# Performance work log

Measured on AMD Instinct MI355X. Metric: run time of the kernel, lower is better.

## Reference

```python
import jax, jax.numpy as jnp
import numpy as np
import math

EMBED = 1024
HEADS = 16
HEAD_DIM = EMBED // HEADS
WINDOW = 128
B, S = 2, 2048


def setup_inputs() -> dict:
    key = jax.random.key(0)
    k1, k2, k3, k4 = jax.random.split(key, 4)
    values = jax.random.normal(k1, (B, S, EMBED), dtype=jnp.float32)
    keys = jax.random.normal(k2, (B, S, EMBED), dtype=jnp.float32)
    queries = jax.random.normal(k3, (B, S, EMBED), dtype=jnp.float32)
    # sliding-window band mask: 1 where |i-j| <= WINDOW//2, else 0
    idx = jnp.arange(S)
    band = (jnp.abs(idx[:, None] - idx[None, :]) <= WINDOW // 2).astype(jnp.int32)
    mask = band[None, None, :, :]  # [1,1,S,S], broadcasts over batch and heads
    w_out = jax.random.normal(k4, (EMBED, EMBED), dtype=jnp.float32) * (1.0 / math.sqrt(EMBED))
    b_out = jnp.zeros((EMBED,), dtype=jnp.float32)
    return {"values": values, "keys": keys, "queries": queries, "mask": mask,
            "w_out": w_out, "b_out": b_out}


def reference(values, keys, queries, mask, w_out, b_out):
    N, q_len = queries.shape[0], queries.shape[1]
    v = values.reshape(N, -1, HEADS, HEAD_DIM)
    k = keys.reshape(N, -1, HEADS, HEAD_DIM)
    q = queries.reshape(N, -1, HEADS, HEAD_DIM)
    # dense N x N energy, as in the original (no windowed blocking)
    energy = jnp.einsum('nqhd,nkhd->nhqk', q, k)
    energy = jnp.where(mask == 0, jnp.float32(-1e20), energy)
    attn = jax.nn.softmax(energy / math.sqrt(EMBED), axis=3)
    out = jnp.einsum('nhql,nlhd->nqhd', attn, v).reshape(N, q_len, HEADS * HEAD_DIM)
    return out @ w_out.T + b_out
```

## Files before the change

### kernel.cpp

```cpp
#include <hip/hip_runtime.h>

typedef __bf16 bf16x8 __attribute__((ext_vector_type(8)));
typedef float floatx4 __attribute__((ext_vector_type(4)));
typedef unsigned short ushortx8 __attribute__((ext_vector_type(8)));
typedef unsigned short ushortx4 __attribute__((ext_vector_type(4)));
typedef unsigned short ushort_t;

#define SB 2048
#define EB 1024
#define HB 16
#define DB 64
#define QT 128
#define KB2 256
#define KROW 72
#define VROW 272
#define PROW 168

__device__ __forceinline__ ushort_t f2bf(float f) {
    union { float f; unsigned int u; } v; v.f = f;
    unsigned int r = v.u + 0x7fffu + ((v.u >> 16) & 1u);
    return (ushort_t)(r >> 16);
}

union BF8 { ushortx8 u; bf16x8 b; };

__global__ __launch_bounds__(256) void cvtw_kernel(const float* __restrict__ w,
                                                   ushort_t* __restrict__ wb) {
    int i = blockIdx.x * 256 + threadIdx.x;
    const float4 v = ((const float4*)w)[i];
    ushortx4 o;
    o.x = f2bf(v.x); o.y = f2bf(v.y); o.z = f2bf(v.z); o.w = f2bf(v.w);
    ((ushortx4*)wb)[i] = o;
}

__global__ __launch_bounds__(512) void attn_kernel(const float* __restrict__ Vg,
                                                   const float* __restrict__ Kg,
                                                   const float* __restrict__ Qg,
                                                   ushort_t* __restrict__ Xg) {
    __shared__ ushort_t KP[8 * 16 * PROW];
    __shared__ ushort_t Vt[DB * VROW];

    const int tid  = threadIdx.x;
    const int wave = tid >> 6;
    const int lane = tid & 63;
    const int l15  = lane & 15;
    const int l4   = lane >> 4;

    const int qt = blockIdx.x & 15;
    const int h  = (blockIdx.x >> 4) & 15;
    const int b  = blockIdx.x >> 8;

    const int q0     = qt * QT;
    const int kstart = q0 - 64;

    const float* Kbase = Kg + ((size_t)b * SB) * EB + h * DB;
    const float* Vbase = Vg + ((size_t)b * SB) * EB + h * DB;

    #pragma unroll
    for (int it = 0; it < (KB2 * DB / 4) / 512; ++it) {
        int idx = it * 512 + tid;
        int j   = idx >> 4;
        int d4  = (idx & 15) * 4;
        int kk  = kstart + j;
        float4 kv = make_float4(0.f, 0.f, 0.f, 0.f);
        float4 vv = make_float4(0.f, 0.f, 0.f, 0.f);
        if (kk >= 0 && kk < SB) {
            kv = *(const float4*)(Kbase + (size_t)kk * EB + d4);
            vv = *(const float4*)(Vbase + (size_t)kk * EB + d4);
        }
        ushortx4 ku;
        ku.x = f2bf(kv.x); ku.y = f2bf(kv.y); ku.z = f2bf(kv.z); ku.w = f2bf(kv.w);
        *(ushortx4*)(KP + j * KROW + d4) = ku;
        Vt[(d4 + 0) * VROW + j] = f2bf(vv.x);
        Vt[(d4 + 1) * VROW + j] = f2bf(vv.y);
        Vt[(d4 + 2) * VROW + j] = f2bf(vv.z);
        Vt[(d4 + 3) * VROW + j] = f2bf(vv.w);
    }
    {
        int r = tid >> 3, c = 256 + ((tid & 7) * 2);
        if (r < DB) { Vt[r * VROW + c] = 0; Vt[r * VROW + c + 1] = 0; }
    }

    const int qrow = q0 + wave * 16 + l15;
    const float* Qrow = Qg + ((size_t)b * SB + qrow) * EB + h * DB;
    bf16x8 qfrag[2];
    #pragma unroll
    for (int ks = 0; ks < 2; ++ks) {
        const float4* p = (const float4*)(Qrow + ks * 32 + l4 * 8);
        float4 a0 = p[0], a1 = p[1];
        BF8 t;
        t.u[0] = f2bf(a0.x); t.u[1] = f2bf(a0.y); t.u[2] = f2bf(a0.z); t.u[3] = f2bf(a0.w);
        t.u[4] = f2bf(a1.x); t.u[5] = f2bf(a1.y); t.u[6] = f2bf(a1.z); t.u[7] = f2bf(a1.w);
        qfrag[ks] = t.b;
    }

    __syncthreads();

    floatx4 sfrag[9];
    #pragma unroll
    for (int nt = 0; nt < 9; ++nt) {
        floatx4 acc = {0.f, 0.f, 0.f, 0.f};
        #pragma unroll
        for (int ks = 0; ks < 2; ++ks) {
            bf16x8 kf = *(const bf16x8*)(KP + (16 * (wave + nt) + l15) * KROW + ks * 32 + l4 * 8);
            acc = __builtin_amdgcn_mfma_f32_16x16x32_bf16(qfrag[ks], kf, acc, 0, 0, 0);
        }
        sfrag[nt] = acc;
    }

    const float scale2 = 0.04508421903306637f;
    #pragma unroll
    for (int nt = 0; nt < 9; ++nt) {
        int key = kstart + 16 * (wave + nt) + l15;
        #pragma unroll
        for (int r = 0; r < 4; ++r) {
            int m = l4 * 4 + r;
            int d = 16 * nt + l15 - m;
            bool valid = (d >= 0) && (d <= 128) && (key >= 0) && (key < SB);
            float s = sfrag[nt][r] * scale2;
            sfrag[nt][r] = valid ? s : -1e30f;
        }
    }
    #pragma unroll
    for (int r = 0; r < 4; ++r) {
        float mx = -1e30f;
        #pragma unroll
        for (int nt = 0; nt < 9; ++nt) mx = fmaxf(mx, sfrag[nt][r]);
        mx = fmaxf(mx, __shfl_xor(mx, 1));
        mx = fmaxf(mx, __shfl_xor(mx, 2));
        mx = fmaxf(mx, __shfl_xor(mx, 4));
        mx = fmaxf(mx, __shfl_xor(mx, 8));
        float sum = 0.f;
        #pragma unroll
        for (int nt = 0; nt < 9; ++nt) {
            float e = exp2f(sfrag[nt][r] - mx);
            sfrag[nt][r] = e;
            sum += e;
        }
        sum += __shfl_xor(sum, 1);
        sum += __shfl_xor(sum, 2);
        sum += __shfl_xor(sum, 4);
        sum += __shfl_xor(sum, 8);
        float inv = 1.f / sum;
        #pragma unroll
        for (int nt = 0; nt < 9; ++nt) sfrag[nt][r] *= inv;
    }

    __syncthreads();
    ushort_t* Pw = KP + wave * (16 * PROW);
    #pragma unroll
    for (int nt = 0; nt < 9; ++nt)
        #pragma unroll
        for (int r = 0; r < 4; ++r)
            Pw[(l4 * 4 + r) * PROW + nt * 16 + l15] = f2bf(sfrag[nt][r]);
    #pragma unroll
    for (int r = 0; r < 4; ++r) {
        int row = l4 * 4 + r;
        if (l15 < 12) {
            Pw[row * PROW + 144 + l15 * 2]     = 0;
            Pw[row * PROW + 144 + l15 * 2 + 1] = 0;
        }
    }
    __syncthreads();

    #pragma unroll
    for (int nt = 0; nt < 4; ++nt) {
        floatx4 acc = {0.f, 0.f, 0.f, 0.f};
        #pragma unroll
        for (int ks = 0; ks < 5; ++ks) {
            bf16x8 pf = *(const bf16x8*)(Pw + l15 * PROW + ks * 32 + l4 * 8);
            bf16x8 vf = *(const bf16x8*)(Vt + (nt * 16 + l15) * VROW + 16 * wave + ks * 32 + l4 * 8);
            acc = __builtin_amdgcn_mfma_f32_16x16x32_bf16(pf, vf, acc, 0, 0, 0);
        }
        #pragma unroll
        for (int r = 0; r < 4; ++r) {
            int q  = q0 + wave * 16 + l4 * 4 + r;
            int dd = h * DB + nt * 16 + l15;
            Xg[((size_t)b * SB + q) * EB + dd] = f2bf(acc[r]);
        }
    }
}

__device__ __forceinline__ void async_load16(const void* g, void* l) {
    __builtin_amdgcn_global_load_lds((__attribute__((address_space(1))) void*)g,
                                     (__attribute__((address_space(3))) void*)l,
                                     16, 0, 0);
}

__global__ __launch_bounds__(256) void proj_kernel(const ushort_t* __restrict__ X,
                                                   const ushort_t* __restrict__ Wb,
                                                   const float* __restrict__ bias,
                                                   float* __restrict__ out) {
    __shared__ ushort_t As[64 * 32];
    __shared__ ushort_t Bs[128 * 32];

    const int tid  = threadIdx.x;
    const int wave = tid >> 6;
    const int lane = tid & 63;
    const int l15  = lane & 15;
    const int l4   = lane >> 4;

    const int m0 = blockIdx.x * 64;
    const int n0 = blockIdx.y * 128;
    const int wm = (wave >> 1) * 32;
    const int wn = (wave & 1) * 64;

    floatx4 acc[2][4];
    #pragma unroll
    for (int i = 0; i < 2; ++i)
        #pragma unroll
        for (int j = 0; j < 4; ++j)
            acc[i][j] = (floatx4){0.f, 0.f, 0.f, 0.f};

    const int cA  = wave * 64 + lane;
    const int cB0 = wave * 128 + lane;
    const ushort_t* gA  = X  + (size_t)(m0 + (cA >> 2)) * EB + (cA & 3) * 8;
    const ushort_t* gB0 = Wb + (size_t)(n0 + (cB0 >> 2)) * EB + (cB0 & 3) * 8;
    const ushort_t* gB1 = Wb + (size_t)(n0 + ((cB0 + 64) >> 2)) * EB + ((cB0 + 64) & 3) * 8;
    ushort_t* lA  = As + wave * 512;
    ushort_t* lB0 = Bs + wave * 1024;
    ushort_t* lB1 = Bs + wave * 1024 + 512;

    for (int kt = 0; kt < EB / 32; ++kt) {
        async_load16(gA,  lA);
        async_load16(gB0, lB0);
        async_load16(gB1, lB1);
        gA += 32; gB0 += 32; gB1 += 32;
        __syncthreads();

        bf16x8 af[2], bfr[4];
        #pragma unroll
        for (int i = 0; i < 2; ++i)
            af[i] = *(const bf16x8*)(As + (wm + i * 16 + l15) * 32 + l4 * 8);
        #pragma unroll
        for (int j = 0; j < 4; ++j)
            bfr[j] = *(const bf16x8*)(Bs + (wn + j * 16 + l15) * 32 + l4 * 8);
        #pragma unroll
        for (int i = 0; i < 2; ++i)
            #pragma unroll
            for (int j = 0; j < 4; ++j)
                acc[i][j] = __builtin_amdgcn_mfma_f32_16x16x32_bf16(af[i], bfr[j], acc[i][j], 0, 0, 0);
        __syncthreads();
    }

    #pragma unroll
    for (int i = 0; i < 2; ++i)
        #pragma unroll
        for (int j = 0; j < 4; ++j)
            #pragma unroll
            for (int r = 0; r < 4; ++r) {
                int row = m0 + wm + i * 16 + l4 * 4 + r;
                int col = n0 + wn + j * 16 + l15;
                out[(size_t)row * EB + col] = acc[i][j][r] + bias[col];
            }
}

extern "C" void kernel_launch(void* const* d_in, const int* in_sizes, int n_in,
                              void* d_out, int out_size, void* d_ws, size_t ws_size,
                              hipStream_t stream) {
    const float* values  = (const float*)d_in[0];
    const float* keys    = (const float*)d_in[1];
    const float* queries = (const float*)d_in[2];
    const float* w_out   = (const float*)d_in[4];
    const float* b_out   = (const float*)d_in[5];
    float* out = (float*)d_out;

    ushort_t* Xb = (ushort_t*)d_ws;
    ushort_t* Wb = (ushort_t*)d_ws + (size_t)4096 * 1024;

    cvtw_kernel<<<(EB * EB / 4) / 256, 256, 0, stream>>>(w_out, Wb);
    attn_kernel<<<2 * HB * (SB / QT), 512, 0, stream>>>(values, keys, queries, Xb);
    proj_kernel<<<dim3(4096 / 64, EB / 128), 256, 0, stream>>>(Xb, Wb, b_out, out);
}
```

Before: 137.2 us.

## Swizzle V tile in LDS, stage attention output through LDS, retile projection GEMM

The attention kernel now XOR-swizzles the transposed V tile in LDS to cut bank conflicts. It also stages each block's output in LDS so it can be written to global memory as coalesced 16-byte stores instead of scattered 2-byte stores. The projection GEMM is retiled to 128x64 tiles with 2 waves, each computing a 64x64 sub-tile, and uses a 64-wide K step with swizzled async LDS loads to cut bank conflicts and barrier count. The trade-off is fewer threads per block, more registers per wave and lower occupancy in the GEMM.

```diff
diff --git a/kernel.cpp b/kernel.cpp
--- a/kernel.cpp
+++ b/kernel.cpp
@@ -15,6 +15,7 @@
 #define KROW 72
 #define VROW 272
 #define PROW 168
+#define XROW 72
 
 __device__ __forceinline__ ushort_t f2bf(float f) {
     union { float f; unsigned int u; } v; v.f = f;
@@ -71,10 +72,11 @@
         ushortx4 ku;
         ku.x = f2bf(kv.x); ku.y = f2bf(kv.y); ku.z = f2bf(kv.z); ku.w = f2bf(kv.w);
         *(ushortx4*)(KP + j * KROW + d4) = ku;
-        Vt[(d4 + 0) * VROW + j] = f2bf(vv.x);
-        Vt[(d4 + 1) * VROW + j] = f2bf(vv.y);
-        Vt[(d4 + 2) * VROW + j] = f2bf(vv.z);
-        Vt[(d4 + 3) * VROW + j] = f2bf(vv.w);
+        int cs = ((((j >> 3) ^ (l15 & 7)) << 3) | (j & 7));
+        Vt[(d4 + 0) * VROW + cs] = f2bf(vv.x);
+        Vt[(d4 + 1) * VROW + cs] = f2bf(vv.y);
+        Vt[(d4 + 2) * VROW + cs] = f2bf(vv.z);
+        Vt[(d4 + 3) * VROW + cs] = f2bf(vv.w);
     }
     {
         int r = tid >> 3, c = 256 + ((tid & 7) * 2);
@@ -161,23 +163,38 @@
             Pw[row * PROW + 144 + l15 * 2 + 1] = 0;
         }
     }
-    __syncthreads();
-
+
+    floatx4 oacc[4];
     #pragma unroll
     for (int nt = 0; nt < 4; ++nt) {
         floatx4 acc = {0.f, 0.f, 0.f, 0.f};
+        int dsw = (nt * 4 + (l15 >> 2)) & 7;
         #pragma unroll
         for (int ks = 0; ks < 5; ++ks) {
+            int col = 16 * wave + ks * 32 + l4 * 8;
+            int c   = col >> 3;
+            int coff = (c < 32) ? ((c ^ dsw) << 3) : (c << 3);
             bf16x8 pf = *(const bf16x8*)(Pw + l15 * PROW + ks * 32 + l4 * 8);
-            bf16x8 vf = *(const bf16x8*)(Vt + (nt * 16 + l15) * VROW + 16 * wave + ks * 32 + l4 * 8);
+            bf16x8 vf = *(const bf16x8*)(Vt + (nt * 16 + l15) * VROW + coff);
             acc = __builtin_amdgcn_mfma_f32_16x16x32_bf16(pf, vf, acc, 0, 0, 0);
         }
-        #pragma unroll
-        for (int r = 0; r < 4; ++r) {
-            int q  = q0 + wave * 16 + l4 * 4 + r;
-            int dd = h * DB + nt * 16 + l15;
-            Xg[((size_t)b * SB + q) * EB + dd] = f2bf(acc[r]);
-        }
+        oacc[nt] = acc;
+    }
+
+    __syncthreads();
+    ushort_t* Xs = KP;
+    #pragma unroll
+    for (int nt = 0; nt < 4; ++nt)
+        #pragma unroll
+        for (int r = 0; r < 4; ++r)
+            Xs[(wave * 16 + l4 * 4 + r) * XROW + nt * 16 + l15] = f2bf(oacc[nt][r]);
+    __syncthreads();
+    #pragma unroll
+    for (int it = 0; it < 2; ++it) {
+        int idx = it * 512 + tid;
+        int row = idx >> 3, ch = idx & 7;
+        bf16x8 val = *(const bf16x8*)(Xs + row * XROW + ch * 8);
+        *(bf16x8*)(Xg + ((size_t)b * SB + q0 + row) * EB + h * DB + ch * 8) = val;
     }
 }
 
@@ -187,12 +204,12 @@
                                      16, 0, 0);
 }
 
-__global__ __launch_bounds__(256) void proj_kernel(const ushort_t* __restrict__ X,
+__global__ __launch_bounds__(128) void proj_kernel(const ushort_t* __restrict__ X,
                                                    const ushort_t* __restrict__ Wb,
                                                    const float* __restrict__ bias,
                                                    float* __restrict__ out) {
-    __shared__ ushort_t As[64 * 32];
-    __shared__ ushort_t Bs[128 * 32];
+    __shared__ ushort_t As[128 * 64];
+    __shared__ ushort_t Bs[64 * 64];
 
     const int tid  = threadIdx.x;
     const int wave = tid >> 6;
@@ -200,59 +217,62 @@
     const int l15  = lane & 15;
     const int l4   = lane >> 4;
 
-    const int m0 = blockIdx.x * 64;
-    const int n0 = blockIdx.y * 128;
-    const int wm = (wave >> 1) * 32;
-    const int wn = (wave & 1) * 64;
-
-    floatx4 acc[2][4];
-    #pragma unroll
-    for (int i = 0; i < 2; ++i)
+    const int m0 = blockIdx.x * 128;
+    const int n0 = blockIdx.y * 64;
+    const int wm = wave * 64;
+
+    floatx4 acc[4][4];
+    #pragma unroll
+    for (int i = 0; i < 4; ++i)
         #pragma unroll
         for (int j = 0; j < 4; ++j)
             acc[i][j] = (floatx4){0.f, 0.f, 0.f, 0.f};
 
-    const int cA  = wave * 64 + lane;
-    const int cB0 = wave * 128 + lane;
-    const ushort_t* gA  = X  + (size_t)(m0 + (cA >> 2)) * EB + (cA & 3) * 8;
-    const ushort_t* gB0 = Wb + (size_t)(n0 + (cB0 >> 2)) * EB + (cB0 & 3) * 8;
-    const ushort_t* gB1 = Wb + (size_t)(n0 + ((cB0 + 64) >> 2)) * EB + ((cB0 + 64) & 3) * 8;
-    ushort_t* lA  = As + wave * 512;
-    ushort_t* lB0 = Bs + wave * 1024;
-    ushort_t* lB1 = Bs + wave * 1024 + 512;
-
-    for (int kt = 0; kt < EB / 32; ++kt) {
-        async_load16(gA,  lA);
-        async_load16(gB0, lB0);
-        async_load16(gB1, lB1);
-        gA += 32; gB0 += 32; gB1 += 32;
+    const int kc8 = (((tid & 7) ^ ((tid >> 3) & 7)) << 3);
+    const ushort_t* gA = X  + (size_t)(m0 + (tid >> 3)) * EB + kc8;
+    const ushort_t* gB = Wb + (size_t)(n0 + (tid >> 3)) * EB + kc8;
+    ushort_t* lA = As + wave * 512;
+    ushort_t* lB = Bs + wave * 512;
+
+    for (int kt = 0; kt < EB / 64; ++kt) {
+        #pragma unroll
+        for (int p = 0; p < 8; ++p) async_load16(gA + (size_t)p * 16 * EB, lA + p * 1024);
+        #pragma unroll
+        for (int p = 0; p < 4; ++p) async_load16(gB + (size_t)p * 16 * EB, lB + p * 1024);
+        gA += 64; gB += 64;
         __syncthreads();
 
-        bf16x8 af[2], bfr[4];
-        #pragma unroll
-        for (int i = 0; i < 2; ++i)
-            af[i] = *(const bf16x8*)(As + (wm + i * 16 + l15) * 32 + l4 * 8);
-        #pragma unroll
-        for (int j = 0; j < 4; ++j)
-            bfr[j] = *(const bf16x8*)(Bs + (wn + j * 16 + l15) * 32 + l4 * 8);
-        #pragma unroll
-        for (int i = 0; i < 2; ++i)
+        #pragma unroll
+        for (int ks = 0; ks < 2; ++ks) {
+            const int sw = (((ks * 4 + l4) ^ (l15 & 7)) << 3);
+            bf16x8 af[4], bfr[4];
+            #pragma unroll
+            for (int i = 0; i < 4; ++i)
+                af[i] = *(const bf16x8*)(As + (wm + i * 16 + l15) * 64 + sw);
             #pragma unroll
             for (int j = 0; j < 4; ++j)
-                acc[i][j] = __builtin_amdgcn_mfma_f32_16x16x32_bf16(af[i], bfr[j], acc[i][j], 0, 0, 0);
+                bfr[j] = *(const bf16x8*)(Bs + (j * 16 + l15) * 64 + sw);
+            #pragma unroll
+            for (int i = 0; i < 4; ++i)
+                #pragma unroll
+                for (int j = 0; j < 4; ++j)
+                    acc[i][j] = __builtin_amdgcn_mfma_f32_16x16x32_bf16(af[i], bfr[j], acc[i][j], 0, 0, 0);
+        }
         __syncthreads();
     }
 
     #pragma unroll
-    for (int i = 0; i < 2; ++i)
-        #pragma unroll
-        for (int j = 0; j < 4; ++j)
+    for (int j = 0; j < 4; ++j) {
+        int col = n0 + j * 16 + l15;
+        float bv = bias[col];
+        #pragma unroll
+        for (int i = 0; i < 4; ++i)
             #pragma unroll
             for (int r = 0; r < 4; ++r) {
                 int row = m0 + wm + i * 16 + l4 * 4 + r;
-                int col = n0 + wn + j * 16 + l15;
-                out[(size_t)row * EB + col] = acc[i][j][r] + bias[col];
+                out[(size_t)row * EB + col] = acc[i][j][r] + bv;
             }
+    }
 }
 
 extern "C" void kernel_launch(void* const* d_in, const int* in_sizes, int n_in,
@@ -270,5 +290,5 @@
 
     cvtw_kernel<<<(EB * EB / 4) / 256, 256, 0, stream>>>(w_out, Wb);
     attn_kernel<<<2 * HB * (SB / QT), 512, 0, stream>>>(values, keys, queries, Xb);
-    proj_kernel<<<dim3(4096 / 64, EB / 128), 256, 0, stream>>>(Xb, Wb, b_out, out);
-}
+    proj_kernel<<<dim3(4096 / 128, EB / 64), 128, 0, stream>>>(Xb, Wb, b_out, out);
+}
```

Result: no change. 137.8 us (+0.4%).
